# Kernel tuning notes

Hardware: AMD Instinct MI355X
Metric: run time of the kernel (lower is better)

Reference implementation:

```python
import jax, jax.numpy as jnp
import numpy as np

B, L, S, E, H = 2, 2048, 2048, 1024, 16
D = E // H


def setup_inputs() -> dict:
    key = jax.random.key(0)
    ks = jax.random.split(key, 16)
    p = 0.02  # small init scale for weights
    return {
        "a": jax.random.normal(ks[0], (B, L, E), jnp.float32),
        "b": jax.random.normal(ks[1], (B, S, E), jnp.float32),
        "Wa_qk": jax.random.normal(ks[2], (E, E), jnp.float32) * p,
        "ba_qk": jax.random.normal(ks[3], (E,), jnp.float32) * p,
        "Wa_v": jax.random.normal(ks[4], (E, E), jnp.float32) * p,
        "ba_v": jax.random.normal(ks[5], (E,), jnp.float32) * p,
        "Wb_qk": jax.random.normal(ks[6], (E, E), jnp.float32) * p,
        "bb_qk": jax.random.normal(ks[7], (E,), jnp.float32) * p,
        "Wb_v": jax.random.normal(ks[8], (E, E), jnp.float32) * p,
        "bb_v": jax.random.normal(ks[9], (E,), jnp.float32) * p,
        "Wa_o": jax.random.normal(ks[10], (E, E), jnp.float32) * p,
        "ba_o": jax.random.normal(ks[11], (E,), jnp.float32) * p,
        "Wb_o": jax.random.normal(ks[12], (E, E), jnp.float32) * p,
        "bb_o": jax.random.normal(ks[13], (E,), jnp.float32) * p,
    }


def _heads(x, n, W, bias):
    # x: [B, N, E] -> projected and split to [B, H, N, D]
    y = x @ W + bias
    return y.reshape(B, n, H, D).transpose(0, 2, 1, 3)


def reference(a, b, Wa_qk, ba_qk, Wa_v, ba_v, Wb_qk, bb_qk, Wb_v, bb_v,
              Wa_o, ba_o, Wb_o, bb_o):
    aq = _heads(a, L, Wa_qk, ba_qk)   # [B,H,L,D]
    av = _heads(a, L, Wa_v, ba_v)     # [B,H,L,D]
    bq = _heads(b, S, Wb_qk, bb_qk)   # [B,H,S,D]
    bv = _heads(b, S, Wb_v, bb_v)     # [B,H,S,D]

    scale = 1.0 / jnp.sqrt(jnp.float32(D))
    # Shared score matrix [B,H,L,S]
    scores = jnp.einsum('bhld,bhsd->bhls', aq, bq) * scale
    # Dual softmax: row-wise (over S) and column-wise (over L)
    wa = jax.nn.softmax(scores, axis=-1)                    # [B,H,L,S]
    wb = jax.nn.softmax(scores, axis=-2).transpose(0, 1, 3, 2)  # [B,H,S,L]

    a_ctx = jnp.einsum('bhls,bhsd->bhld', wa, bv)  # [B,H,L,D]
    b_ctx = jnp.einsum('bhsl,bhld->bhsd', wb, av)  # [B,H,S,D]

    a_out = a_ctx.transpose(0, 2, 1, 3).reshape(B, L, E) @ Wa_o + ba_o
    b_out = b_ctx.transpose(0, 2, 1, 3).reshape(B, S, E) @ Wb_o + bb_o
    return (a_out, b_out)
```

## Files before the change

### kernel.cpp

```cpp
#include <hip/hip_runtime.h>
#include <hip/hip_bf16.h>
#include <stdint.h>

typedef unsigned short u16;
typedef __attribute__((ext_vector_type(8))) short bf16x8;
typedef __attribute__((ext_vector_type(4))) float f32x4;

typedef __attribute__((address_space(3))) void lds_void;
typedef const __attribute__((address_space(1))) void gbl_void;

#define SIDE 4194304u
#define BHSTR 131072u

static __device__ __forceinline__ u16 f2bf(float f) {
  union { __hip_bfloat16 b; u16 u; } cv;
  cv.b = __float2bfloat16(f);
  return cv.u;
}
static __device__ __forceinline__ float bf2f(u16 u) {
  union { __hip_bfloat16 b; u16 u; } cv;
  cv.u = u;
  return __bfloat162float(cv.b);
}

__global__ __launch_bounds__(256) void k_cvt_in(const float* __restrict__ a,
                                                const float* __restrict__ b,
                                                u16* __restrict__ dst) {
  int z = blockIdx.y;
  const float* src = z ? b : a;
  size_t i = ((size_t)blockIdx.x * 256 + threadIdx.x) * 8;
  float4 x0 = *(const float4*)(src + i);
  float4 x1 = *(const float4*)(src + i + 4);
  u16 t[8] = {f2bf(x0.x), f2bf(x0.y), f2bf(x0.z), f2bf(x0.w),
              f2bf(x1.x), f2bf(x1.y), f2bf(x1.z), f2bf(x1.w)};
  *(uint4*)(dst + (size_t)z * SIDE + i) = *(uint4*)t;
}

__global__ __launch_bounds__(256) void k_cvt_bias(
    const float* s0, const float* s1, const float* s2, const float* s3,
    const float* s4, const float* s5, u16* __restrict__ dst) {
  const float* srcs[6] = {s0, s1, s2, s3, s4, s5};
  int z = blockIdx.y;
  int i = blockIdx.x * 256 + threadIdx.x;
  float sc = (z == 0) ? 0.125f : 1.0f;
  dst[z * 1024 + i] = f2bf(srcs[z][i] * sc);
}

__global__ __launch_bounds__(256) void k_transpose_w(
    const float* a0, const float* a1, const float* a2, const float* a3,
    const float* a4, const float* a5,
    u16* d0, u16* d1, u16* d2, u16* d3, u16* d4, u16* d5) {
  __shared__ u16 tile[64][72];
  const float* srcs[6] = {a0, a1, a2, a3, a4, a5};
  u16* dsts[6] = {d0, d1, d2, d3, d4, d5};
  int z = blockIdx.z;
  float sc = (z == 0) ? 0.125f : 1.0f;
  const float* src = srcs[z] + (size_t)(blockIdx.y * 64) * 1024 + blockIdx.x * 64;
  int t = threadIdx.x;
  int row = t >> 2, c4 = t & 3;
#pragma unroll
  for (int p = 0; p < 2; ++p) {
    int col = c4 * 8 + p * 32;
    const float* sf = src + (size_t)row * 1024 + col;
    float4 x0 = *(const float4*)sf;
    float4 x1 = *(const float4*)(sf + 4);
    u16 tmp[8] = {f2bf(x0.x * sc), f2bf(x0.y * sc), f2bf(x0.z * sc), f2bf(x0.w * sc),
                  f2bf(x1.x * sc), f2bf(x1.y * sc), f2bf(x1.z * sc), f2bf(x1.w * sc)};
    *(uint4*)(&tile[row][col]) = *(uint4*)tmp;
  }
  __syncthreads();
  u16* dst = dsts[z] + (size_t)(blockIdx.x * 64) * 1024 + blockIdx.y * 64;
#pragma unroll
  for (int p = 0; p < 2; ++p) {
    int col = c4 * 8 + p * 32;
    u16 tmp[8];
#pragma unroll
    for (int i = 0; i < 8; ++i) tmp[i] = tile[col + i][row];
    *(uint4*)(dst + (size_t)row * 1024 + col) = *(uint4*)tmp;
  }
}

__global__ __launch_bounds__(256) void k_gemm_qkv(
    const u16* __restrict__ Aall, const u16* __restrict__ WtA,
    const u16* __restrict__ WtB, const u16* __restrict__ bias,
    u16* __restrict__ qkbuf, u16* __restrict__ vbuf) {
  __shared__ u16 As[128 * 32];
  __shared__ u16 Bs[128 * 32];
  int tid = threadIdx.x;
  int wave = tid >> 6, lane = tid & 63;
  int quad = lane >> 4, lrow = lane & 15;
  int wr = wave >> 1, wc = wave & 1;
  int z = blockIdx.z;
  int m0 = blockIdx.y * 128, n0 = blockIdx.x * 128;
  const u16* A = Aall + (size_t)z * SIDE;
  const u16* Wt = z ? WtB : WtA;
  const u16* bi = bias + (size_t)z * 2048;

  f32x4 acc[4][4] = {};
  int srow = 32 * wave + (lane >> 2);
  int scol = (lane & 3) * 8;
  const u16* gA = A + (size_t)(m0 + srow) * 1024 + scol;
  const u16* gB = Wt + (size_t)(n0 + srow) * 1024 + scol;
  u16* lA = &As[(32 * wave) * 32];
  u16* lB = &Bs[(32 * wave) * 32];

  for (int k0 = 0; k0 < 1024; k0 += 32) {
    __syncthreads();
#pragma unroll
    for (int j = 0; j < 2; ++j) {
      __builtin_amdgcn_global_load_lds((gbl_void*)(gA + (size_t)(16 * j) * 1024 + k0),
                                       (lds_void*)(lA + 16 * j * 32), 16, 0, 0);
      __builtin_amdgcn_global_load_lds((gbl_void*)(gB + (size_t)(16 * j) * 1024 + k0),
                                       (lds_void*)(lB + 16 * j * 32), 16, 0, 0);
    }
    __syncthreads();
    bf16x8 af[4], bfr[4];
#pragma unroll
    for (int i = 0; i < 4; ++i)
      af[i] = *(const bf16x8*)&As[(64 * wr + 16 * i + lrow) * 32 + 8 * quad];
#pragma unroll
    for (int j = 0; j < 4; ++j)
      bfr[j] = *(const bf16x8*)&Bs[(64 * wc + 16 * j + lrow) * 32 + 8 * quad];
#pragma unroll
    for (int i = 0; i < 4; ++i)
#pragma unroll
      for (int j = 0; j < 4; ++j)
        acc[i][j] = __builtin_amdgcn_mfma_f32_16x16x32_bf16(af[i], bfr[j], acc[i][j], 0, 0, 0);
  }

  int x = blockIdx.x;
  bool isv = (x >= 8);
  int h = (isv ? 2 * (x - 8) : 2 * x) + wc;
  u16* dst = (isv ? vbuf : qkbuf) + (size_t)z * SIDE;

  float bv[4];
#pragma unroll
  for (int j = 0; j < 4; ++j) bv[j] = bf2f(bi[n0 + 64 * wc + 16 * j + lrow]);

#pragma unroll
  for (int i = 0; i < 4; ++i) {
    int row0 = m0 + 64 * wr + 16 * i + 4 * quad;
#pragma unroll
    for (int r = 0; r < 4; ++r) {
      int rg = row0 + r;
      int bb = rg >> 11, rl = rg & 2047;
      u16* dr = dst + (size_t)(bb * 16 + h) * BHSTR + (size_t)rl * 64;
#pragma unroll
      for (int j = 0; j < 4; ++j)
        dr[16 * j + lrow] = f2bf(acc[i][j][r] + bv[j]);
    }
  }
}

__global__ __launch_bounds__(256) void k_transpose_v(const u16* __restrict__ v,
                                                     u16* __restrict__ vt) {
  __shared__ u16 tile[64][72];
  int sbh = blockIdx.y;
  int n0 = blockIdx.x * 64;
  const u16* src = v + (size_t)sbh * BHSTR + (size_t)n0 * 64;
  u16* dst = vt + (size_t)sbh * BHSTR + n0;
  int t = threadIdx.x;
  int row = t >> 2, c4 = t & 3;
#pragma unroll
  for (int p = 0; p < 2; ++p) {
    int col = c4 * 8 + p * 32;
    uint4 q = *(const uint4*)(src + (size_t)row * 64 + col);
    *(uint4*)(&tile[row][col]) = q;
  }
  __syncthreads();
#pragma unroll
  for (int p = 0; p < 2; ++p) {
    int col = c4 * 8 + p * 32;
    u16 tmp[8];
#pragma unroll
    for (int i = 0; i < 8; ++i) tmp[i] = tile[col + i][row];
    *(uint4*)(dst + (size_t)row * 2048 + col) = *(uint4*)tmp;
  }
}

__global__ __launch_bounds__(256) void k_attn(
    const u16* __restrict__ qk, const u16* __restrict__ vt,
    u16* __restrict__ ctx) {
  __shared__ u16 Ks[64 * 64];
  __shared__ u16 Vs[64 * 64];
  __shared__ u16 Ps[128 * 72];
  int tid = threadIdx.x;
  int wave = tid >> 6, lane = tid & 63;
  int quad = lane >> 4, lrow = lane & 15;
  int z = blockIdx.z, bh = blockIdx.y;
  int l0 = blockIdx.x * 128;
  const u16* Qb = qk + (size_t)z * SIDE + (size_t)bh * BHSTR + (size_t)l0 * 64;
  const u16* Kb = qk + (size_t)(1 - z) * SIDE + (size_t)bh * BHSTR;
  const u16* Vtb = vt + (size_t)(1 - z) * SIDE + (size_t)bh * BHSTR;

#pragma unroll
  for (int p = 0; p < 4; ++p) {
    int G0 = wave * 256 + p * 64;
    int G = G0 + lane;
    int row = G >> 3, c = G & 7;
    const u16* src = Qb + (size_t)row * 64 + ((c ^ (row & 7)) * 8);
    __builtin_amdgcn_global_load_lds((gbl_void*)src, (lds_void*)(Ps + G0 * 8), 16, 0, 0);
  }
  __syncthreads();
  bf16x8 qf[2][2];
#pragma unroll
  for (int rt = 0; rt < 2; ++rt) {
    int lq = 32 * wave + 16 * rt + lrow;
    qf[rt][0] = *(const bf16x8*)&Ps[(lq * 8 + (quad ^ (lq & 7))) * 8];
    qf[rt][1] = *(const bf16x8*)&Ps[(lq * 8 + ((quad + 4) ^ (lq & 7))) * 8];
  }

  f32x4 cacc[2][4] = {};
  float rsum[2][4] = {};

  for (int s0 = 0; s0 < 2048; s0 += 64) {
    __syncthreads();
#pragma unroll
    for (int p = 0; p < 2; ++p) {
      int G0 = p * 256 + wave * 64;
      int G = G0 + lane;
      int row = G >> 3, c = G & 7;
      int sw = (c ^ (row & 7)) * 8;
      __builtin_amdgcn_global_load_lds((gbl_void*)(Kb + (size_t)(s0 + row) * 64 + sw),
                                       (lds_void*)(Ks + G0 * 8), 16, 0, 0);
      __builtin_amdgcn_global_load_lds((gbl_void*)(Vtb + (size_t)row * 2048 + s0 + sw),
                                       (lds_void*)(Vs + G0 * 8), 16, 0, 0);
    }
    __syncthreads();
#pragma unroll
    for (int j = 0; j < 4; ++j) {
      int kr = 16 * j + lrow;
      bf16x8 kf0 = *(const bf16x8*)&Ks[(kr * 8 + (quad ^ (kr & 7))) * 8];
      bf16x8 kf1 = *(const bf16x8*)&Ks[(kr * 8 + ((quad + 4) ^ (kr & 7))) * 8];
#pragma unroll
      for (int rt = 0; rt < 2; ++rt) {
        f32x4 s = {};
        s = __builtin_amdgcn_mfma_f32_16x16x32_bf16(qf[rt][0], kf0, s, 0, 0, 0);
        s = __builtin_amdgcn_mfma_f32_16x16x32_bf16(qf[rt][1], kf1, s, 0, 0, 0);
        u16* pp = &Ps[(32 * wave + 16 * rt + 4 * quad) * 72 + lrow];
#pragma unroll
        for (int r = 0; r < 4; ++r) {
          float pv = __expf(s[r]);
          rsum[rt][r] += pv;
          pp[r * 72 + 16 * j] = f2bf(pv);
        }
      }
    }
    asm volatile("s_waitcnt lgkmcnt(0)" ::: "memory");
    bf16x8 pf[2][2];
#pragma unroll
    for (int rt = 0; rt < 2; ++rt) {
      const u16* q = &Ps[(32 * wave + 16 * rt + lrow) * 72];
      pf[rt][0] = *(const bf16x8*)(q + 8 * quad);
      pf[rt][1] = *(const bf16x8*)(q + 32 + 8 * quad);
    }
#pragma unroll
    for (int j = 0; j < 4; ++j) {
      int vr = 16 * j + lrow;
      bf16x8 vf0 = *(const bf16x8*)&Vs[(vr * 8 + (quad ^ (vr & 7))) * 8];
      bf16x8 vf1 = *(const bf16x8*)&Vs[(vr * 8 + ((quad + 4) ^ (vr & 7))) * 8];
#pragma unroll
      for (int rt = 0; rt < 2; ++rt) {
        cacc[rt][j] = __builtin_amdgcn_mfma_f32_16x16x32_bf16(pf[rt][0], vf0, cacc[rt][j], 0, 0, 0);
        cacc[rt][j] = __builtin_amdgcn_mfma_f32_16x16x32_bf16(pf[rt][1], vf1, cacc[rt][j], 0, 0, 0);
      }
    }
  }

  float rinv[2][4];
#pragma unroll
  for (int rt = 0; rt < 2; ++rt)
#pragma unroll
    for (int r = 0; r < 4; ++r) {
      float v = rsum[rt][r];
      v += __shfl_xor(v, 1);
      v += __shfl_xor(v, 2);
      v += __shfl_xor(v, 4);
      v += __shfl_xor(v, 8);
      rinv[rt][r] = 1.0f / v;
    }

  int bb = bh >> 4, h = bh & 15;
  u16* Ob = ctx + (size_t)z * SIDE + (size_t)(bb * 2048 + l0) * 1024 + h * 64;
#pragma unroll
  for (int rt = 0; rt < 2; ++rt)
#pragma unroll
    for (int r = 0; r < 4; ++r) {
      int l = 32 * wave + 16 * rt + 4 * quad + r;
#pragma unroll
      for (int j = 0; j < 4; ++j)
        Ob[(size_t)l * 1024 + 16 * j + lrow] = f2bf(cacc[rt][j][r] * rinv[rt][r]);
    }
}

__global__ __launch_bounds__(256) void k_gemm_o(
    const u16* __restrict__ ctx, const u16* __restrict__ WtO,
    const u16* __restrict__ bias, float* __restrict__ out) {
  __shared__ u16 As[128 * 32];
  __shared__ u16 Bs[128 * 32];
  int tid = threadIdx.x;
  int wave = tid >> 6, lane = tid & 63;
  int quad = lane >> 4, lrow = lane & 15;
  int wr = wave >> 1, wc = wave & 1;
  int z = blockIdx.z;
  int m0 = blockIdx.y * 128, n0 = blockIdx.x * 128;
  const u16* A = ctx + (size_t)z * SIDE;
  const u16* Wt = WtO + (size_t)z * 1048576;
  const u16* bi = bias + (size_t)z * 1024;
  float* C = out + (size_t)z * SIDE;

  f32x4 acc[4][4] = {};
  int srow = 32 * wave + (lane >> 2);
  int scol = (lane & 3) * 8;
  const u16* gA = A + (size_t)(m0 + srow) * 1024 + scol;
  const u16* gB = Wt + (size_t)(n0 + srow) * 1024 + scol;
  u16* lA = &As[(32 * wave) * 32];
  u16* lB = &Bs[(32 * wave) * 32];

  for (int k0 = 0; k0 < 1024; k0 += 32) {
    __syncthreads();
#pragma unroll
    for (int j = 0; j < 2; ++j) {
      __builtin_amdgcn_global_load_lds((gbl_void*)(gA + (size_t)(16 * j) * 1024 + k0),
                                       (lds_void*)(lA + 16 * j * 32), 16, 0, 0);
      __builtin_amdgcn_global_load_lds((gbl_void*)(gB + (size_t)(16 * j) * 1024 + k0),
                                       (lds_void*)(lB + 16 * j * 32), 16, 0, 0);
    }
    __syncthreads();
    bf16x8 af[4], bfr[4];
#pragma unroll
    for (int i = 0; i < 4; ++i)
      af[i] = *(const bf16x8*)&As[(64 * wr + 16 * i + lrow) * 32 + 8 * quad];
#pragma unroll
    for (int j = 0; j < 4; ++j)
      bfr[j] = *(const bf16x8*)&Bs[(64 * wc + 16 * j + lrow) * 32 + 8 * quad];
#pragma unroll
    for (int i = 0; i < 4; ++i)
#pragma unroll
      for (int j = 0; j < 4; ++j)
        acc[i][j] = __builtin_amdgcn_mfma_f32_16x16x32_bf16(af[i], bfr[j], acc[i][j], 0, 0, 0);
  }

  float bv[4];
#pragma unroll
  for (int j = 0; j < 4; ++j) bv[j] = bf2f(bi[n0 + 64 * wc + 16 * j + lrow]);
#pragma unroll
  for (int i = 0; i < 4; ++i) {
    int row = m0 + 64 * wr + 16 * i + 4 * quad;
#pragma unroll
    for (int j = 0; j < 4; ++j) {
      int col = n0 + 64 * wc + 16 * j + lrow;
#pragma unroll
      for (int r = 0; r < 4; ++r)
        C[(size_t)(row + r) * 1024 + col] = acc[i][j][r] + bv[j];
    }
  }
}

extern "C" void kernel_launch(void* const* d_in, const int* in_sizes, int n_in,
                              void* d_out, int out_size, void* d_ws, size_t ws_size,
                              hipStream_t stream) {
  (void)in_sizes; (void)n_in; (void)out_size; (void)ws_size;
  const size_t M1 = 1048576u;
  u16* ws = (u16*)d_ws;
  u16* wtA   = ws;
  u16* wtB   = ws + 2 * M1;
  u16* wtO   = ws + 4 * M1;
  u16* biasQ = ws + 6 * M1;
  u16* biasO = ws + 6 * M1 + 4096;
  u16* ab    = ws + 7 * M1;
  u16* vt    = ab;
  u16* qkbuf = ws + 15 * M1;
  u16* vbuf  = ws + 23 * M1;
  u16* ctx   = vbuf;

  dim3 blk(256);
  k_cvt_in<<<dim3(2048, 2), blk, 0, stream>>>((const float*)d_in[0],
                                              (const float*)d_in[1], ab);
  k_cvt_bias<<<dim3(4, 6), blk, 0, stream>>>(
      (const float*)d_in[3], (const float*)d_in[5], (const float*)d_in[7],
      (const float*)d_in[9], (const float*)d_in[11], (const float*)d_in[13], biasQ);
  k_transpose_w<<<dim3(16, 16, 6), blk, 0, stream>>>(
      (const float*)d_in[2], (const float*)d_in[4], (const float*)d_in[6],
      (const float*)d_in[8], (const float*)d_in[10], (const float*)d_in[12],
      wtA, wtA + M1, wtB, wtB + M1, wtO, wtO + M1);
  k_gemm_qkv<<<dim3(16, 32, 2), blk, 0, stream>>>(ab, wtA, wtB, biasQ, qkbuf, vbuf);
  k_transpose_v<<<dim3(32, 64), blk, 0, stream>>>(vbuf, vt);
  k_attn<<<dim3(16, 32, 2), blk, 0, stream>>>(qkbuf, vt, ctx);
  k_gemm_o<<<dim3(8, 32, 2), blk, 0, stream>>>(ctx, wtO, biasO, (float*)d_out);
}
```

Baseline: 317.6 us.

## Double-buffer K/V tiles in attention, transpose score MFMA, stage QKV epilogue via LDS

The attention kernel now double-buffers its K and V tiles and prefetches the next tile before computing on the current one, so global-to-LDS loads overlap with MFMA work and one barrier per iteration goes away. The score MFMA operands are swapped, so each lane holds four consecutive S values. These are packed and written as one 8-byte store into an XOR-swizzled, unpadded P buffer, and the row-sum reduction becomes a cross-quad shuffle. The grid axes are swapped so consecutive blocks walk L-tiles in a different order, which may change L2 reuse of K and V. The QKV GEMM epilogue stages results through LDS so each lane issues 16-byte coalesced global stores instead of scattered 2-byte ones, at the cost of extra LDS traffic and a barrier.

```diff
diff --git a/kernel.cpp b/kernel.cpp
--- a/kernel.cpp
+++ b/kernel.cpp
@@ -3,6 +3,7 @@
 #include <stdint.h>
 
 typedef unsigned short u16;
+typedef unsigned int u32;
 typedef __attribute__((ext_vector_type(8))) short bf16x8;
 typedef __attribute__((ext_vector_type(4))) float f32x4;
 
@@ -84,8 +85,9 @@
     const u16* __restrict__ Aall, const u16* __restrict__ WtA,
     const u16* __restrict__ WtB, const u16* __restrict__ bias,
     u16* __restrict__ qkbuf, u16* __restrict__ vbuf) {
-  __shared__ u16 As[128 * 32];
-  __shared__ u16 Bs[128 * 32];
+  __shared__ u16 Sh[8192];
+  u16* As = Sh;
+  u16* Bs = Sh + 4096;
   int tid = threadIdx.x;
   int wave = tid >> 6, lane = tid & 63;
   int quad = lane >> 4, lrow = lane & 15;
@@ -128,27 +130,38 @@
         acc[i][j] = __builtin_amdgcn_mfma_f32_16x16x32_bf16(af[i], bfr[j], acc[i][j], 0, 0, 0);
   }
 
+  float bv[4];
+#pragma unroll
+  for (int j = 0; j < 4; ++j) bv[j] = bf2f(bi[n0 + 64 * wc + 16 * j + lrow]);
+
   int x = blockIdx.x;
   bool isv = (x >= 8);
   int h = (isv ? 2 * (x - 8) : 2 * x) + wc;
   u16* dst = (isv ? vbuf : qkbuf) + (size_t)z * SIDE;
-
-  float bv[4];
-#pragma unroll
-  for (int j = 0; j < 4; ++j) bv[j] = bf2f(bi[n0 + 64 * wc + 16 * j + lrow]);
-
+  u16* lw = Sh + wave * 1216;
+
+  __syncthreads();
 #pragma unroll
   for (int i = 0; i < 4; ++i) {
-    int row0 = m0 + 64 * wr + 16 * i + 4 * quad;
-#pragma unroll
-    for (int r = 0; r < 4; ++r) {
-      int rg = row0 + r;
-      int bb = rg >> 11, rl = rg & 2047;
-      u16* dr = dst + (size_t)(bb * 16 + h) * BHSTR + (size_t)rl * 64;
-#pragma unroll
-      for (int j = 0; j < 4; ++j)
-        dr[16 * j + lrow] = f2bf(acc[i][j][r] + bv[j]);
-    }
+#pragma unroll
+    for (int j = 0; j < 4; ++j)
+#pragma unroll
+      for (int r = 0; r < 4; ++r)
+        lw[(4 * quad + r) * 76 + 16 * j + lrow] = f2bf(acc[i][j][r] + bv[j]);
+    asm volatile("s_waitcnt lgkmcnt(0)" ::: "memory");
+    int row = lane >> 2, cg = (lane & 3) * 16;
+    int rg = m0 + 64 * wr + 16 * i + row;
+    int bb = rg >> 11, rl = rg & 2047;
+    u16* dr = dst + (size_t)(bb * 16 + h) * BHSTR + (size_t)rl * 64 + cg;
+    uint2 w0 = *(const uint2*)&lw[row * 76 + cg];
+    uint2 w1 = *(const uint2*)&lw[row * 76 + cg + 4];
+    uint2 w2 = *(const uint2*)&lw[row * 76 + cg + 8];
+    uint2 w3 = *(const uint2*)&lw[row * 76 + cg + 12];
+    uint4 o0 = {w0.x, w0.y, w1.x, w1.y};
+    uint4 o1 = {w2.x, w2.y, w3.x, w3.y};
+    *(uint4*)dr = o0;
+    *(uint4*)(dr + 8) = o1;
+    asm volatile("s_waitcnt lgkmcnt(0)" ::: "memory");
   }
 }
 
@@ -181,14 +194,14 @@
 __global__ __launch_bounds__(256) void k_attn(
     const u16* __restrict__ qk, const u16* __restrict__ vt,
     u16* __restrict__ ctx) {
-  __shared__ u16 Ks[64 * 64];
-  __shared__ u16 Vs[64 * 64];
-  __shared__ u16 Ps[128 * 72];
+  __shared__ u16 Ks[2 * 4096];
+  __shared__ u16 Vs[2 * 4096];
+  __shared__ u16 Ps[128 * 64];
   int tid = threadIdx.x;
   int wave = tid >> 6, lane = tid & 63;
   int quad = lane >> 4, lrow = lane & 15;
-  int z = blockIdx.z, bh = blockIdx.y;
-  int l0 = blockIdx.x * 128;
+  int z = blockIdx.z, bh = blockIdx.x;
+  int l0 = blockIdx.y * 128;
   const u16* Qb = qk + (size_t)z * SIDE + (size_t)bh * BHSTR + (size_t)l0 * 64;
   const u16* Kb = qk + (size_t)(1 - z) * SIDE + (size_t)bh * BHSTR;
   const u16* Vtb = vt + (size_t)(1 - z) * SIDE + (size_t)bh * BHSTR;
@@ -198,67 +211,86 @@
     int G0 = wave * 256 + p * 64;
     int G = G0 + lane;
     int row = G >> 3, c = G & 7;
-    const u16* src = Qb + (size_t)row * 64 + ((c ^ (row & 7)) * 8);
-    __builtin_amdgcn_global_load_lds((gbl_void*)src, (lds_void*)(Ps + G0 * 8), 16, 0, 0);
-  }
-  __syncthreads();
+    __builtin_amdgcn_global_load_lds((gbl_void*)(Qb + (size_t)row * 64 + ((c ^ (row & 7)) * 8)),
+                                     (lds_void*)(Ps + G0 * 8), 16, 0, 0);
+  }
+#pragma unroll
+  for (int p = 0; p < 2; ++p) {
+    int G0 = p * 256 + wave * 64;
+    int G = G0 + lane;
+    int row = G >> 3, c = G & 7;
+    int sw = (c ^ (row & 7)) * 8;
+    __builtin_amdgcn_global_load_lds((gbl_void*)(Kb + (size_t)row * 64 + sw),
+                                     (lds_void*)(Ks + G0 * 8), 16, 0, 0);
+    __builtin_amdgcn_global_load_lds((gbl_void*)(Vtb + (size_t)row * 2048 + sw),
+                                     (lds_void*)(Vs + G0 * 8), 16, 0, 0);
+  }
+
   bf16x8 qf[2][2];
-#pragma unroll
-  for (int rt = 0; rt < 2; ++rt) {
-    int lq = 32 * wave + 16 * rt + lrow;
-    qf[rt][0] = *(const bf16x8*)&Ps[(lq * 8 + (quad ^ (lq & 7))) * 8];
-    qf[rt][1] = *(const bf16x8*)&Ps[(lq * 8 + ((quad + 4) ^ (lq & 7))) * 8];
-  }
-
   f32x4 cacc[2][4] = {};
-  float rsum[2][4] = {};
-
-  for (int s0 = 0; s0 < 2048; s0 += 64) {
+  float rsum[2] = {0.f, 0.f};
+  int e = 2 * (lrow & 7);
+
+  for (int it = 0; it < 32; ++it) {
     __syncthreads();
-#pragma unroll
-    for (int p = 0; p < 2; ++p) {
-      int G0 = p * 256 + wave * 64;
-      int G = G0 + lane;
-      int row = G >> 3, c = G & 7;
-      int sw = (c ^ (row & 7)) * 8;
-      __builtin_amdgcn_global_load_lds((gbl_void*)(Kb + (size_t)(s0 + row) * 64 + sw),
-                                       (lds_void*)(Ks + G0 * 8), 16, 0, 0);
-      __builtin_amdgcn_global_load_lds((gbl_void*)(Vtb + (size_t)row * 2048 + s0 + sw),
-                                       (lds_void*)(Vs + G0 * 8), 16, 0, 0);
-    }
-    __syncthreads();
+    if (it == 0) {
+#pragma unroll
+      for (int rt = 0; rt < 2; ++rt) {
+        int lq = 32 * wave + 16 * rt + lrow;
+        qf[rt][0] = *(const bf16x8*)&Ps[(lq * 8 + (quad ^ (lq & 7))) * 8];
+        qf[rt][1] = *(const bf16x8*)&Ps[(lq * 8 + ((quad + 4) ^ (lq & 7))) * 8];
+      }
+    }
+    int prty = it & 1;
+    if (it + 1 < 32) {
+      int s1 = (it + 1) << 6;
+      int nb = (1 - prty) * 4096;
+#pragma unroll
+      for (int p = 0; p < 2; ++p) {
+        int G0 = p * 256 + wave * 64;
+        int G = G0 + lane;
+        int row = G >> 3, c = G & 7;
+        int sw = (c ^ (row & 7)) * 8;
+        __builtin_amdgcn_global_load_lds((gbl_void*)(Kb + (size_t)(s1 + row) * 64 + sw),
+                                         (lds_void*)(Ks + nb + G0 * 8), 16, 0, 0);
+        __builtin_amdgcn_global_load_lds((gbl_void*)(Vtb + (size_t)row * 2048 + s1 + sw),
+                                         (lds_void*)(Vs + nb + G0 * 8), 16, 0, 0);
+      }
+    }
+    const u16* KsC = Ks + prty * 4096;
+    const u16* VsC = Vs + prty * 4096;
 #pragma unroll
     for (int j = 0; j < 4; ++j) {
       int kr = 16 * j + lrow;
-      bf16x8 kf0 = *(const bf16x8*)&Ks[(kr * 8 + (quad ^ (kr & 7))) * 8];
-      bf16x8 kf1 = *(const bf16x8*)&Ks[(kr * 8 + ((quad + 4) ^ (kr & 7))) * 8];
+      bf16x8 kf0 = *(const bf16x8*)&KsC[(kr * 8 + (quad ^ (kr & 7))) * 8];
+      bf16x8 kf1 = *(const bf16x8*)&KsC[(kr * 8 + ((quad + 4) ^ (kr & 7))) * 8];
 #pragma unroll
       for (int rt = 0; rt < 2; ++rt) {
         f32x4 s = {};
-        s = __builtin_amdgcn_mfma_f32_16x16x32_bf16(qf[rt][0], kf0, s, 0, 0, 0);
-        s = __builtin_amdgcn_mfma_f32_16x16x32_bf16(qf[rt][1], kf1, s, 0, 0, 0);
-        u16* pp = &Ps[(32 * wave + 16 * rt + 4 * quad) * 72 + lrow];
-#pragma unroll
-        for (int r = 0; r < 4; ++r) {
-          float pv = __expf(s[r]);
-          rsum[rt][r] += pv;
-          pp[r * 72 + 16 * j] = f2bf(pv);
-        }
+        s = __builtin_amdgcn_mfma_f32_16x16x32_bf16(kf0, qf[rt][0], s, 0, 0, 0);
+        s = __builtin_amdgcn_mfma_f32_16x16x32_bf16(kf1, qf[rt][1], s, 0, 0, 0);
+        float e0 = __expf(s[0]), e1 = __expf(s[1]);
+        float e2 = __expf(s[2]), e3 = __expf(s[3]);
+        rsum[rt] += (e0 + e1) + (e2 + e3);
+        uint2 pk;
+        pk.x = ((u32)f2bf(e1) << 16) | (u32)f2bf(e0);
+        pk.y = ((u32)f2bf(e3) << 16) | (u32)f2bf(e2);
+        *(uint2*)&Ps[(32 * wave + 16 * rt + lrow) * 64 + ((4 * j + quad) ^ e) * 4] = pk;
       }
     }
     asm volatile("s_waitcnt lgkmcnt(0)" ::: "memory");
     bf16x8 pf[2][2];
 #pragma unroll
     for (int rt = 0; rt < 2; ++rt) {
-      const u16* q = &Ps[(32 * wave + 16 * rt + lrow) * 72];
-      pf[rt][0] = *(const bf16x8*)(q + 8 * quad);
-      pf[rt][1] = *(const bf16x8*)(q + 32 + 8 * quad);
+      const u16* pr = &Ps[(32 * wave + 16 * rt + lrow) * 64];
+      pf[rt][0] = *(const bf16x8*)&pr[((2 * quad) ^ e) * 4];
+      pf[rt][1] = *(const bf16x8*)&pr[((2 * quad + 8) ^ e) * 4];
     }
 #pragma unroll
     for (int j = 0; j < 4; ++j) {
       int vr = 16 * j + lrow;
-      bf16x8 vf0 = *(const bf16x8*)&Vs[(vr * 8 + (quad ^ (vr & 7))) * 8];
-      bf16x8 vf1 = *(const bf16x8*)&Vs[(vr * 8 + ((quad + 4) ^ (vr & 7))) * 8];
+      bf16x8 vf0 = *(const bf16x8*)&VsC[(vr * 8 + (quad ^ (vr & 7))) * 8];
+      bf16x8 vf1 = *(const bf16x8*)&VsC[(vr * 8 + ((quad + 4) ^ (vr & 7))) * 8];
 #pragma unroll
       for (int rt = 0; rt < 2; ++rt) {
         cacc[rt][j] = __builtin_amdgcn_mfma_f32_16x16x32_bf16(pf[rt][0], vf0, cacc[rt][j], 0, 0, 0);
@@ -269,16 +301,15 @@
 
   float rinv[2][4];
 #pragma unroll
-  for (int rt = 0; rt < 2; ++rt)
-#pragma unroll
-    for (int r = 0; r < 4; ++r) {
-      float v = rsum[rt][r];
-      v += __shfl_xor(v, 1);
-      v += __shfl_xor(v, 2);
-      v += __shfl_xor(v, 4);
-      v += __shfl_xor(v, 8);
-      rinv[rt][r] = 1.0f / v;
-    }
+  for (int rt = 0; rt < 2; ++rt) {
+    float v = rsum[rt];
+    v += __shfl_xor(v, 16);
+    v += __shfl_xor(v, 32);
+    float rv = 1.0f / v;
+#pragma unroll
+    for (int r = 0; r < 4; ++r)
+      rinv[rt][r] = __shfl(rv, 20 * quad + r);
+  }
 
   int bb = bh >> 4, h = bh & 15;
   u16* Ob = ctx + (size_t)z * SIDE + (size_t)(bb * 2048 + l0) * 1024 + h * 64;
@@ -386,6 +417,6 @@
       wtA, wtA + M1, wtB, wtB + M1, wtO, wtO + M1);
   k_gemm_qkv<<<dim3(16, 32, 2), blk, 0, stream>>>(ab, wtA, wtB, biasQ, qkbuf, vbuf);
   k_transpose_v<<<dim3(32, 64), blk, 0, stream>>>(vbuf, vt);
-  k_attn<<<dim3(16, 32, 2), blk, 0, stream>>>(qkbuf, vt, ctx);
+  k_attn<<<dim3(32, 16, 2), blk, 0, stream>>>(qkbuf, vt, ctx);
   k_gemm_o<<<dim3(8, 32, 2), blk, 0, stream>>>(ctx, wtO, biasO, (float*)d_out);
 }
```

New measurement: 315.1 us. No clear change (-0.8%).
